# Kernel optimization log

Hardware: AMD Instinct MI355X
Metric: run time of the kernel (lower is better)

Reference implementation:

```python
import jax, jax.numpy as jnp
import numpy as np

B, V, H, R, RULE_DIM, DK, GMLP_H, OUT = 4096, 8, 512, 16, 64, 32, 16, 512
TEMP = float(np.sqrt(DK))  # SelectAttention temperature = sqrt(d_k)
EPS = 1e-10


def gumbel_hard(logits, u, tau=1.0):
    # straight-through hard gumbel-softmax over last axis (F.gumbel_softmax hard=True)
    g = -jnp.log(-jnp.log(u + EPS) + EPS)
    y = jax.nn.softmax((logits + g) / tau, axis=-1)
    hard = jax.nn.one_hot(jnp.argmax(y, axis=-1), y.shape[-1], dtype=y.dtype)
    return hard + y - jax.lax.stop_gradient(y)


def setup_inputs() -> dict:
    key = jax.random.key(0)
    ks = jax.random.split(key, 16)
    s = lambda d: 1.0 / np.sqrt(d)
    return {
        "hidden": jax.random.normal(ks[0], (B, V, H), jnp.float32),
        "u_var": jax.random.uniform(ks[1], (B, V * V), jnp.float32),
        "u_rule": jax.random.uniform(ks[2], (B, R), jnp.float32),
        # variable_rule_select: shared query/key Linear(H, 32)
        "Wq": jax.random.normal(ks[3], (H, DK), jnp.float32) * s(H),
        "bq": jnp.zeros((DK,), jnp.float32),
        "Wk": jax.random.normal(ks[4], (H, DK), jnp.float32) * s(H),
        "bk": jnp.zeros((DK,), jnp.float32),
        # rule embeddings [R, rule_dim]
        "rule_emb": jax.random.normal(ks[5], (R, RULE_DIM), jnp.float32),
        # rule_select_: shared Linear(3H, 32) query, Linear(rule_dim, 32) key
        "Wq2": jax.random.normal(ks[6], (3 * H, DK), jnp.float32) * s(3 * H),
        "bq2": jnp.zeros((DK,), jnp.float32),
        "Wk2": jax.random.normal(ks[7], (RULE_DIM, DK), jnp.float32) * s(RULE_DIM),
        "bk2": jnp.zeros((DK,), jnp.float32),
        # rule_mlp = GroupMLP(2H -> 16 -> input_dim, num=R), GroupLinearLayer has no bias
        "W1": jax.random.normal(ks[8], (R, 2 * H, GMLP_H), jnp.float32) * s(2 * H),
        "W2": jax.random.normal(ks[9], (R, GMLP_H, OUT), jnp.float32) * s(GMLP_H),
    }


def reference(hidden, u_var, u_rule, Wq, bq, Wk, bk, rule_emb, Wq2, bq2, Wk2, bk2, W1, W2):
    b, v, h = hidden.shape
    # variable_rule_select(hidden, hidden): shared Linear projections, bmm scores
    q = hidden @ Wq + bq                                  # [B,V,dk]
    k = hidden @ Wk + bk                                  # [B,V,dk]
    scores = jnp.einsum('bid,bjd->bij', q, k) / TEMP      # [B,V,V]
    # hard gumbel-softmax over flattened V*V pair grid
    mask = gumbel_hard(scores.reshape(b, -1), u_var).reshape(b, v, v)
    mask = mask.transpose(0, 2, 1)                        # mask.permute(0,2,1)
    primary = mask.sum(axis=2)                            # [B,V] one-hot primary variable
    context = mask.sum(axis=1)                            # [B,V] one-hot context variable
    h_p = jnp.einsum('bv,bvh->bh', primary, hidden)       # gather primary slot
    h_c = jnp.einsum('bv,bvh->bh', context, hidden)       # gather context slot
    h_mean = hidden.mean(axis=1)
    # rule_select_: query from concat(primary, context, pooled state) [B,3H]
    q2 = jnp.concatenate([h_p, h_c, h_mean], axis=-1) @ Wq2 + bq2   # [B,dk]
    k2 = rule_emb @ Wk2 + bk2                                        # [R,dk]
    rscores = (q2 @ k2.T) / TEMP                                     # [B,R]
    rmask = gumbel_hard(rscores, u_rule)                             # [B,R] one-hot rule
    # rule_mlp: GroupMLP(2H->16->input_dim) over all rules, then hard dispatch
    comb = jnp.concatenate([h_p, h_c], axis=-1)                      # [B,2H]
    h1 = jax.nn.relu(jnp.einsum('bd,rde->bre', comb, W1))            # [B,R,16]
    rout = jnp.einsum('bre,reo->bro', h1, W2)                        # [B,R,out]
    rule_out = jnp.einsum('br,bro->bo', rmask, rout)                 # [B,out]
    # scatter result back to the selected primary variable slot
    out = primary[:, :, None] * rule_out[:, None, :]                 # [B,V,out]
    return out
```

## Files before the change

### kernel.cpp

```cpp
#include <hip/hip_runtime.h>

#define TEMP 5.656854249492380195f
#define EPSG 1e-10f

#define XSTR 68
#define WSTR 64

__launch_bounds__(256, 2)
__global__ void k1_kernel(const float* __restrict__ hidden,
                          const float* __restrict__ u_var,
                          const float* __restrict__ Wq,
                          const float* __restrict__ bq,
                          const float* __restrict__ Wk,
                          const float* __restrict__ bk,
                          const float* __restrict__ rule_emb,
                          const float* __restrict__ Wk2,
                          const float* __restrict__ bk2,
                          float* __restrict__ k2f,
                          int* __restrict__ selbuf,
                          float* __restrict__ outbuf) {
    const int tid = threadIdx.x;
    const int b0  = blockIdx.x * 8;

    __shared__ float4 smem4[(64 * XSTR + 64 * WSTR) / 4];
    float* smem = reinterpret_cast<float*>(smem4);
    float* xt = smem;
    float* wt = smem + 64 * XSTR;

    if (blockIdx.x == 0) {
        for (int t = tid; t < 512; t += 256) {
            int r = t >> 5, d = t & 31;
            float acc = bk2[d];
            for (int h = 0; h < 64; ++h)
                acc += rule_emb[r * 64 + h] * Wk2[h * 32 + d];
            k2f[t] = acc;
        }
    }

    const int tn = tid & 15;
    const int tm = tid >> 4;

    float4 acc0 = make_float4(0.f, 0.f, 0.f, 0.f);
    float4 acc1 = make_float4(0.f, 0.f, 0.f, 0.f);
    float4 acc2 = make_float4(0.f, 0.f, 0.f, 0.f);
    float4 acc3 = make_float4(0.f, 0.f, 0.f, 0.f);

    for (int c = 0; c < 8; ++c) {
        #pragma unroll
        for (int p = 0; p < 4; ++p) {
            int f   = p * 256 + tid;
            int row = f >> 4;
            int c4  = f & 15;
            int bb  = row >> 3, v = row & 7;
            float4 val = *reinterpret_cast<const float4*>(
                hidden + (size_t)(b0 + bb) * 4096 + v * 512 + c * 64 + c4 * 4);
            *reinterpret_cast<float4*>(&xt[row * XSTR + c4 * 4]) = val;
        }
        #pragma unroll
        for (int p = 0; p < 4; ++p) {
            int f  = p * 256 + tid;
            int k  = f >> 4;
            int n4 = f & 15;
            int h  = c * 64 + k;
            const float* src = (n4 < 8) ? (Wq + h * 32 + n4 * 4)
                                        : (Wk + h * 32 + (n4 - 8) * 4);
            *reinterpret_cast<float4*>(&wt[k * WSTR + n4 * 4]) =
                *reinterpret_cast<const float4*>(src);
        }
        __syncthreads();

        #pragma unroll 4
        for (int k4 = 0; k4 < 16; ++k4) {
            float4 x0 = *reinterpret_cast<const float4*>(&xt[(tm * 4 + 0) * XSTR + k4 * 4]);
            float4 x1 = *reinterpret_cast<const float4*>(&xt[(tm * 4 + 1) * XSTR + k4 * 4]);
            float4 x2 = *reinterpret_cast<const float4*>(&xt[(tm * 4 + 2) * XSTR + k4 * 4]);
            float4 x3 = *reinterpret_cast<const float4*>(&xt[(tm * 4 + 3) * XSTR + k4 * 4]);
            float4 w0 = *reinterpret_cast<const float4*>(&wt[(k4 * 4 + 0) * WSTR + tn * 4]);
            float4 w1 = *reinterpret_cast<const float4*>(&wt[(k4 * 4 + 1) * WSTR + tn * 4]);
            float4 w2 = *reinterpret_cast<const float4*>(&wt[(k4 * 4 + 2) * WSTR + tn * 4]);
            float4 w3 = *reinterpret_cast<const float4*>(&wt[(k4 * 4 + 3) * WSTR + tn * 4]);
            acc0.x += x0.x * w0.x + x0.y * w1.x + x0.z * w2.x + x0.w * w3.x;
            acc0.y += x0.x * w0.y + x0.y * w1.y + x0.z * w2.y + x0.w * w3.y;
            acc0.z += x0.x * w0.z + x0.y * w1.z + x0.z * w2.z + x0.w * w3.z;
            acc0.w += x0.x * w0.w + x0.y * w1.w + x0.z * w2.w + x0.w * w3.w;
            acc1.x += x1.x * w0.x + x1.y * w1.x + x1.z * w2.x + x1.w * w3.x;
            acc1.y += x1.x * w0.y + x1.y * w1.y + x1.z * w2.y + x1.w * w3.y;
            acc1.z += x1.x * w0.z + x1.y * w1.z + x1.z * w2.z + x1.w * w3.z;
            acc1.w += x1.x * w0.w + x1.y * w1.w + x1.z * w2.w + x1.w * w3.w;
            acc2.x += x2.x * w0.x + x2.y * w1.x + x2.z * w2.x + x2.w * w3.x;
            acc2.y += x2.x * w0.y + x2.y * w1.y + x2.z * w2.y + x2.w * w3.y;
            acc2.z += x2.x * w0.z + x2.y * w1.z + x2.z * w2.z + x2.w * w3.z;
            acc2.w += x2.x * w0.w + x2.y * w1.w + x2.z * w2.w + x2.w * w3.w;
            acc3.x += x3.x * w0.x + x3.y * w1.x + x3.z * w2.x + x3.w * w3.x;
            acc3.y += x3.x * w0.y + x3.y * w1.y + x3.z * w2.y + x3.w * w3.y;
            acc3.z += x3.x * w0.z + x3.y * w1.z + x3.z * w2.z + x3.w * w3.z;
            acc3.w += x3.x * w0.w + x3.y * w1.w + x3.z * w2.w + x3.w * w3.w;
        }

        {
            int bb = tid >> 5, hg = tid & 31;
            float m0 = 0.f, m1 = 0.f;
            #pragma unroll
            for (int v = 0; v < 8; ++v) {
                float2 x2 = *reinterpret_cast<const float2*>(&xt[(bb * 8 + v) * XSTR + hg * 2]);
                m0 += x2.x; m1 += x2.y;
            }
            float2 o; o.x = m0 * 0.125f; o.y = m1 * 0.125f;
            *reinterpret_cast<float2*>(outbuf + (size_t)(b0 + bb) * 4096 + c * 64 + hg * 2) = o;
        }
        __syncthreads();
    }

    {
        const float* bsrc = (tn < 8) ? (bq + tn * 4) : (bk + (tn - 8) * 4);
        float4 bias4 = *reinterpret_cast<const float4*>(bsrc);
        float4 r0, r1, r2, r3;
        r0.x = acc0.x + bias4.x; r0.y = acc0.y + bias4.y; r0.z = acc0.z + bias4.z; r0.w = acc0.w + bias4.w;
        r1.x = acc1.x + bias4.x; r1.y = acc1.y + bias4.y; r1.z = acc1.z + bias4.z; r1.w = acc1.w + bias4.w;
        r2.x = acc2.x + bias4.x; r2.y = acc2.y + bias4.y; r2.z = acc2.z + bias4.z; r2.w = acc2.w + bias4.w;
        r3.x = acc3.x + bias4.x; r3.y = acc3.y + bias4.y; r3.z = acc3.z + bias4.z; r3.w = acc3.w + bias4.w;
        float* sq = smem;
        *reinterpret_cast<float4*>(&sq[(tm * 4 + 0) * XSTR + tn * 4]) = r0;
        *reinterpret_cast<float4*>(&sq[(tm * 4 + 1) * XSTR + tn * 4]) = r1;
        *reinterpret_cast<float4*>(&sq[(tm * 4 + 2) * XSTR + tn * 4]) = r2;
        *reinterpret_cast<float4*>(&sq[(tm * 4 + 3) * XSTR + tn * 4]) = r3;
    }
    __syncthreads();

    {
        const float* sq = smem;
        const int w    = tid >> 6;
        const int lane = tid & 63;
        #pragma unroll
        for (int half = 0; half < 2; ++half) {
            const int bb = w + half * 4;
            const int b  = b0 + bb;
            const int i = lane >> 3, j = lane & 7;
            float s = 0.f;
            #pragma unroll
            for (int d4 = 0; d4 < 8; ++d4) {
                float4 qv = *reinterpret_cast<const float4*>(&sq[(bb * 8 + i) * XSTR + d4 * 4]);
                float4 kv = *reinterpret_cast<const float4*>(&sq[(bb * 8 + j) * XSTR + 32 + d4 * 4]);
                s += qv.x * kv.x + qv.y * kv.y + qv.z * kv.z + qv.w * kv.w;
            }
            s /= TEMP;
            float u = u_var[(size_t)b * 64 + lane];
            float g = -logf(-logf(u + EPSG) + EPSG);
            float pm = s + g;
            int idx = lane;
            #pragma unroll
            for (int off = 32; off >= 1; off >>= 1) {
                float pv = __shfl_xor(pm, off);
                int   pi = __shfl_xor(idx, off);
                if (pv > pm || (pv == pm && pi < idx)) { pm = pv; idx = pi; }
            }
            if (lane == 0) selbuf[b] = idx;
        }
    }
}

__launch_bounds__(256, 4)
__global__ void k2sel_kernel(const float* __restrict__ hidden,
                             const float* __restrict__ u_rule,
                             const float* __restrict__ Wq2,
                             const float* __restrict__ bq2,
                             const float* __restrict__ k2f,
                             const int* __restrict__ selbuf,
                             const float* __restrict__ hmeanbuf,
                             int* __restrict__ rselbuf) {
    const int tid = threadIdx.x;
    const int b0 = blockIdx.x * 8;

    __shared__ float  s_k2[512];
    __shared__ float  xt[8][256];
    __shared__ float4 part4[4][8][8];
    __shared__ float  s_q2[8][32];
    __shared__ int    s_sel8[8];

    s_k2[tid]       = k2f[tid];
    s_k2[tid + 256] = k2f[tid + 256];
    if (tid < 8) s_sel8[tid] = selbuf[b0 + tid];
    __syncthreads();

    const int d4 = tid & 7, s = tid >> 3;
    float4 acc[8];
    #pragma unroll
    for (int bb = 0; bb < 8; ++bb) acc[bb] = make_float4(0.f, 0.f, 0.f, 0.f);

    for (int kt = 0; kt < 6; ++kt) {
        float4 w[8];
        #pragma unroll
        for (int j = 0; j < 8; ++j)
            w[j] = *reinterpret_cast<const float4*>(Wq2 + (size_t)(kt * 256 + s * 8 + j) * 32 + d4 * 4);
        #pragma unroll
        for (int bb = 0; bb < 8; ++bb) {
            const int b  = b0 + bb;
            const int sv = s_sel8[bb];
            const float* src;
            if (kt < 2)      src = hidden  + ((size_t)b * 8 + (sv & 7))  * 512 + kt * 256;
            else if (kt < 4) src = hidden  + ((size_t)b * 8 + (sv >> 3)) * 512 + (kt - 2) * 256;
            else             src = hmeanbuf + (size_t)b * 4096 + (kt - 4) * 256;
            xt[bb][tid] = src[tid];
        }
        __syncthreads();
        #pragma unroll
        for (int bb = 0; bb < 8; ++bb) {
            #pragma unroll
            for (int j = 0; j < 8; ++j) {
                float x = xt[bb][s * 8 + j];
                acc[bb].x += x * w[j].x;
                acc[bb].y += x * w[j].y;
                acc[bb].z += x * w[j].z;
                acc[bb].w += x * w[j].w;
            }
        }
        __syncthreads();
    }
    #pragma unroll
    for (int off = 8; off < 64; off <<= 1) {
        #pragma unroll
        for (int bb = 0; bb < 8; ++bb) {
            acc[bb].x += __shfl_xor(acc[bb].x, off);
            acc[bb].y += __shfl_xor(acc[bb].y, off);
            acc[bb].z += __shfl_xor(acc[bb].z, off);
            acc[bb].w += __shfl_xor(acc[bb].w, off);
        }
    }
    if ((s & 7) == 0) {
        #pragma unroll
        for (int bb = 0; bb < 8; ++bb) part4[tid >> 6][bb][d4] = acc[bb];
    }
    __syncthreads();
    {
        const int bb = tid >> 5, col = tid & 31;
        float q2 = bq2[col];
        #pragma unroll
        for (int wv = 0; wv < 4; ++wv) {
            const float* pf = reinterpret_cast<const float*>(&part4[wv][bb][col >> 2]);
            q2 += pf[col & 3];
        }
        s_q2[bb][col] = q2;
    }
    __syncthreads();
    if (tid < 128) {
        const int bb = tid >> 4, r = tid & 15;
        const int b = b0 + bb;
        float sc = 0.f;
        #pragma unroll
        for (int d = 0; d < 32; ++d) sc += s_q2[bb][d] * s_k2[r * 32 + d];
        sc /= TEMP;
        float u = u_rule[(size_t)b * 16 + r];
        float g = -logf(-logf(u + EPSG) + EPSG);
        float pm = sc + g;
        int idx = r;
        #pragma unroll
        for (int off = 8; off >= 1; off >>= 1) {
            float pv = __shfl_xor(pm, off, 16);
            int   pi = __shfl_xor(idx, off, 16);
            if (pv > pm || (pv == pm && pi < idx)) { pm = pv; idx = pi; }
        }
        if (r == 0) rselbuf[b] = idx;
    }
}

__launch_bounds__(256, 4)
__global__ void k3_kernel(const float* __restrict__ hidden,
                          const float* __restrict__ W1,
                          const float* __restrict__ W2,
                          const int* __restrict__ selbuf,
                          const int* __restrict__ rselbuf,
                          float* __restrict__ outbuf) {
    const int tid = threadIdx.x;
    const int b   = blockIdx.x;

    __shared__ float comb[1024];
    __shared__ float part[4][16];
    __shared__ float s_h1[16];
    __shared__ float s_rout[512];

    const int sv = selbuf[b];
    const int r  = rselbuf[b];
    const int js = sv & 7, cs = sv >> 3;

    {
        const float4* h4 = reinterpret_cast<const float4*>(hidden);
        float4 v;
        if (tid < 128) v = h4[((size_t)b * 8 + js) * 128 + tid];
        else           v = h4[((size_t)b * 8 + cs) * 128 + (tid - 128)];
        *reinterpret_cast<float4*>(&comb[tid * 4]) = v;
    }
    __syncthreads();

    {
        const int e  = tid & 15;
        const int sl = tid >> 4;
        const float* w1p = W1 + (size_t)r * 16384;
        float a = 0.f;
        for (int i = 0; i < 64; ++i) {
            int rr = i * 16 + sl;
            a += comb[rr] * w1p[rr * 16 + e];
        }
        a += __shfl_xor(a, 16);
        a += __shfl_xor(a, 32);
        if ((sl & 3) == 0) part[sl >> 2][e] = a;
    }
    __syncthreads();
    if (tid < 16)
        s_h1[tid] = fmaxf(part[0][tid] + part[1][tid] + part[2][tid] + part[3][tid], 0.f);
    __syncthreads();

    {
        const float* w2 = W2 + (size_t)r * 8192;
        int o0 = tid * 2;
        float a0 = 0.f, a1 = 0.f;
        #pragma unroll
        for (int ee = 0; ee < 16; ++ee) {
            float h1e = s_h1[ee];
            float2 ww = *reinterpret_cast<const float2*>(w2 + ee * 512 + o0);
            a0 += h1e * ww.x;
            a1 += h1e * ww.y;
        }
        s_rout[o0]     = a0;
        s_rout[o0 + 1] = a1;
    }
    __syncthreads();

    {
        const int v    = tid >> 5;
        const int col0 = (tid & 31) * 16;
        float4 z = make_float4(0.f, 0.f, 0.f, 0.f);
        float4 r0 = z, r1 = z, r2 = z, r3 = z;
        if (v == js) {
            r0 = *reinterpret_cast<const float4*>(&s_rout[col0]);
            r1 = *reinterpret_cast<const float4*>(&s_rout[col0 + 4]);
            r2 = *reinterpret_cast<const float4*>(&s_rout[col0 + 8]);
            r3 = *reinterpret_cast<const float4*>(&s_rout[col0 + 12]);
        }
        float* ob = outbuf + (size_t)b * 4096 + v * 512 + col0;
        *reinterpret_cast<float4*>(ob)      = r0;
        *reinterpret_cast<float4*>(ob + 4)  = r1;
        *reinterpret_cast<float4*>(ob + 8)  = r2;
        *reinterpret_cast<float4*>(ob + 12) = r3;
    }
}

extern "C" void kernel_launch(void* const* d_in, const int* in_sizes, int n_in,
                              void* d_out, int out_size, void* d_ws, size_t ws_size,
                              hipStream_t stream) {
    const float* hidden   = (const float*)d_in[0];
    const float* u_var    = (const float*)d_in[1];
    const float* u_rule   = (const float*)d_in[2];
    const float* Wq       = (const float*)d_in[3];
    const float* bq       = (const float*)d_in[4];
    const float* Wk       = (const float*)d_in[5];
    const float* bk       = (const float*)d_in[6];
    const float* rule_emb = (const float*)d_in[7];
    const float* Wq2      = (const float*)d_in[8];
    const float* bq2      = (const float*)d_in[9];
    const float* Wk2      = (const float*)d_in[10];
    const float* bk2      = (const float*)d_in[11];
    const float* W1       = (const float*)d_in[12];
    const float* W2       = (const float*)d_in[13];

    char* ws = (char*)d_ws;
    float* k2f  = (float*)(ws);
    int*   sel  = (int*)(ws + 4096);
    int*   rsel = (int*)(ws + 20480);
    float* outf = (float*)d_out;

    hipLaunchKernelGGL(k1_kernel, dim3(512), dim3(256), 0, stream,
                       hidden, u_var, Wq, bq, Wk, bk,
                       rule_emb, Wk2, bk2, k2f, sel, outf);
    hipLaunchKernelGGL(k2sel_kernel, dim3(512), dim3(256), 0, stream,
                       hidden, u_rule, Wq2, bq2, k2f, sel, outf, rsel);
    hipLaunchKernelGGL(k3_kernel, dim3(4096), dim3(256), 0, stream,
                       hidden, W1, W2, sel, rsel, outf);
}
```

Measured before the change: 91.47 us.

## Register-prefetch next tile in k1 and halve batches per block in k2sel

In k1, the global loads for the next 64-wide chunk of hidden and Wq/Wk are issued into registers before the current chunk's FMA loop, then written to shared memory after the barrier, so memory latency overlaps with compute. k2sel now processes 4 batch rows per block instead of 8 and launches twice as many blocks, which raises parallelism across CUs but re-reads the Wq2 weights twice as often. The prefetch adds registers per thread, which may affect occupancy under the launch bounds of 2.

```diff
diff --git a/kernel.cpp b/kernel.cpp
--- a/kernel.cpp
+++ b/kernel.cpp
@@ -40,34 +40,47 @@
     const int tn = tid & 15;
     const int tm = tid >> 4;
 
+    const int srow = tid >> 4;
+    const int sc4  = tid & 15;
+
     float4 acc0 = make_float4(0.f, 0.f, 0.f, 0.f);
     float4 acc1 = make_float4(0.f, 0.f, 0.f, 0.f);
     float4 acc2 = make_float4(0.f, 0.f, 0.f, 0.f);
     float4 acc3 = make_float4(0.f, 0.f, 0.f, 0.f);
 
+    float4 px[4], pw[4];
+
+    #pragma unroll
+    for (int p = 0; p < 4; ++p) {
+        int row = p * 16 + srow;
+        int bb  = row >> 3, v = row & 7;
+        px[p] = *reinterpret_cast<const float4*>(
+            hidden + (size_t)(b0 + bb) * 4096 + v * 512 + 0 * 64 + sc4 * 4);
+        const float* wsrc = (sc4 < 8) ? (Wq + (0 * 64 + row) * 32 + sc4 * 4)
+                                      : (Wk + (0 * 64 + row) * 32 + (sc4 - 8) * 4);
+        pw[p] = *reinterpret_cast<const float4*>(wsrc);
+    }
+    #pragma unroll
+    for (int p = 0; p < 4; ++p) {
+        int row = p * 16 + srow;
+        *reinterpret_cast<float4*>(&xt[row * XSTR + sc4 * 4]) = px[p];
+        *reinterpret_cast<float4*>(&wt[row * WSTR + sc4 * 4]) = pw[p];
+    }
+    __syncthreads();
+
     for (int c = 0; c < 8; ++c) {
-        #pragma unroll
-        for (int p = 0; p < 4; ++p) {
-            int f   = p * 256 + tid;
-            int row = f >> 4;
-            int c4  = f & 15;
-            int bb  = row >> 3, v = row & 7;
-            float4 val = *reinterpret_cast<const float4*>(
-                hidden + (size_t)(b0 + bb) * 4096 + v * 512 + c * 64 + c4 * 4);
-            *reinterpret_cast<float4*>(&xt[row * XSTR + c4 * 4]) = val;
-        }
-        #pragma unroll
-        for (int p = 0; p < 4; ++p) {
-            int f  = p * 256 + tid;
-            int k  = f >> 4;
-            int n4 = f & 15;
-            int h  = c * 64 + k;
-            const float* src = (n4 < 8) ? (Wq + h * 32 + n4 * 4)
-                                        : (Wk + h * 32 + (n4 - 8) * 4);
-            *reinterpret_cast<float4*>(&wt[k * WSTR + n4 * 4]) =
-                *reinterpret_cast<const float4*>(src);
-        }
-        __syncthreads();
+        if (c < 7) {
+            #pragma unroll
+            for (int p = 0; p < 4; ++p) {
+                int row = p * 16 + srow;
+                int bb  = row >> 3, v = row & 7;
+                px[p] = *reinterpret_cast<const float4*>(
+                    hidden + (size_t)(b0 + bb) * 4096 + v * 512 + (c + 1) * 64 + sc4 * 4);
+                const float* wsrc = (sc4 < 8) ? (Wq + ((c + 1) * 64 + row) * 32 + sc4 * 4)
+                                              : (Wk + ((c + 1) * 64 + row) * 32 + (sc4 - 8) * 4);
+                pw[p] = *reinterpret_cast<const float4*>(wsrc);
+            }
+        }
 
         #pragma unroll 4
         for (int k4 = 0; k4 < 16; ++k4) {
@@ -109,6 +122,16 @@
             *reinterpret_cast<float2*>(outbuf + (size_t)(b0 + bb) * 4096 + c * 64 + hg * 2) = o;
         }
         __syncthreads();
+
+        if (c < 7) {
+            #pragma unroll
+            for (int p = 0; p < 4; ++p) {
+                int row = p * 16 + srow;
+                *reinterpret_cast<float4*>(&xt[row * XSTR + sc4 * 4]) = px[p];
+                *reinterpret_cast<float4*>(&wt[row * WSTR + sc4 * 4]) = pw[p];
+            }
+            __syncthreads();
+        }
     }
 
     {
@@ -169,23 +192,23 @@
                              const float* __restrict__ hmeanbuf,
                              int* __restrict__ rselbuf) {
     const int tid = threadIdx.x;
-    const int b0 = blockIdx.x * 8;
+    const int b0 = blockIdx.x * 4;
 
     __shared__ float  s_k2[512];
-    __shared__ float  xt[8][256];
-    __shared__ float4 part4[4][8][8];
-    __shared__ float  s_q2[8][32];
-    __shared__ int    s_sel8[8];
+    __shared__ float  xt[4][256];
+    __shared__ float4 part4[4][4][8];
+    __shared__ float  s_q2[4][32];
+    __shared__ int    s_sel4[4];
 
     s_k2[tid]       = k2f[tid];
     s_k2[tid + 256] = k2f[tid + 256];
-    if (tid < 8) s_sel8[tid] = selbuf[b0 + tid];
+    if (tid < 4) s_sel4[tid] = selbuf[b0 + tid];
     __syncthreads();
 
     const int d4 = tid & 7, s = tid >> 3;
-    float4 acc[8];
+    float4 acc[4];
     #pragma unroll
-    for (int bb = 0; bb < 8; ++bb) acc[bb] = make_float4(0.f, 0.f, 0.f, 0.f);
+    for (int bb = 0; bb < 4; ++bb) acc[bb] = make_float4(0.f, 0.f, 0.f, 0.f);
 
     for (int kt = 0; kt < 6; ++kt) {
         float4 w[8];
@@ -193,9 +216,9 @@
         for (int j = 0; j < 8; ++j)
             w[j] = *reinterpret_cast<const float4*>(Wq2 + (size_t)(kt * 256 + s * 8 + j) * 32 + d4 * 4);
         #pragma unroll
-        for (int bb = 0; bb < 8; ++bb) {
+        for (int bb = 0; bb < 4; ++bb) {
             const int b  = b0 + bb;
-            const int sv = s_sel8[bb];
+            const int sv = s_sel4[bb];
             const float* src;
             if (kt < 2)      src = hidden  + ((size_t)b * 8 + (sv & 7))  * 512 + kt * 256;
             else if (kt < 4) src = hidden  + ((size_t)b * 8 + (sv >> 3)) * 512 + (kt - 2) * 256;
@@ -204,7 +227,7 @@
         }
         __syncthreads();
         #pragma unroll
-        for (int bb = 0; bb < 8; ++bb) {
+        for (int bb = 0; bb < 4; ++bb) {
             #pragma unroll
             for (int j = 0; j < 8; ++j) {
                 float x = xt[bb][s * 8 + j];
@@ -219,7 +242,7 @@
     #pragma unroll
     for (int off = 8; off < 64; off <<= 1) {
         #pragma unroll
-        for (int bb = 0; bb < 8; ++bb) {
+        for (int bb = 0; bb < 4; ++bb) {
             acc[bb].x += __shfl_xor(acc[bb].x, off);
             acc[bb].y += __shfl_xor(acc[bb].y, off);
             acc[bb].z += __shfl_xor(acc[bb].z, off);
@@ -228,10 +251,10 @@
     }
     if ((s & 7) == 0) {
         #pragma unroll
-        for (int bb = 0; bb < 8; ++bb) part4[tid >> 6][bb][d4] = acc[bb];
-    }
-    __syncthreads();
-    {
+        for (int bb = 0; bb < 4; ++bb) part4[tid >> 6][bb][d4] = acc[bb];
+    }
+    __syncthreads();
+    if (tid < 128) {
         const int bb = tid >> 5, col = tid & 31;
         float q2 = bq2[col];
         #pragma unroll
@@ -242,7 +265,7 @@
         s_q2[bb][col] = q2;
     }
     __syncthreads();
-    if (tid < 128) {
+    if (tid < 64) {
         const int bb = tid >> 4, r = tid & 15;
         const int b = b0 + bb;
         float sc = 0.f;
@@ -371,7 +394,7 @@
     hipLaunchKernelGGL(k1_kernel, dim3(512), dim3(256), 0, stream,
                        hidden, u_var, Wq, bq, Wk, bk,
                        rule_emb, Wk2, bk2, k2f, sel, outf);
-    hipLaunchKernelGGL(k2sel_kernel, dim3(512), dim3(256), 0, stream,
+    hipLaunchKernelGGL(k2sel_kernel, dim3(1024), dim3(256), 0, stream,
                        hidden, u_rule, Wq2, bq2, k2f, sel, outf, rsel);
     hipLaunchKernelGGL(k3_kernel, dim3(4096), dim3(256), 0, stream,
                        hidden, W1, W2, sel, rsel, outf);
```

New measurement: 109.4 us. +19.7%, slower.

## Fuse rule selection and rule MLP into one kernel with per-wave batches

Applied to the files above, without the earlier changes.

Merges the rule-selection kernel and the rule-MLP/scatter kernel into a single kernel that processes 4 batch rows per block. The gathered primary/context rows and the mean state are loaded into shared memory once and reused for both the Wq2 projection and the W1 MLP. Each wave then computes one batch's MLP, broadcasting the hidden activations by shuffle instead of shared memory. This removes a launch, the rsel round trip through global memory and the repeated gather of hidden rows. In exchange it uses more shared memory per block, with a lower occupancy bound, and only 4 rows share each Wq2 weight load instead of 8.

```diff
diff --git a/kernel.cpp b/kernel.cpp
--- a/kernel.cpp
+++ b/kernel.cpp
@@ -159,79 +159,99 @@
     }
 }
 
-__launch_bounds__(256, 4)
-__global__ void k2sel_kernel(const float* __restrict__ hidden,
-                             const float* __restrict__ u_rule,
-                             const float* __restrict__ Wq2,
-                             const float* __restrict__ bq2,
-                             const float* __restrict__ k2f,
-                             const int* __restrict__ selbuf,
-                             const float* __restrict__ hmeanbuf,
-                             int* __restrict__ rselbuf) {
+__launch_bounds__(256, 3)
+__global__ void k23_kernel(const float* __restrict__ hidden,
+                           const float* __restrict__ u_rule,
+                           const float* __restrict__ Wq2,
+                           const float* __restrict__ bq2,
+                           const float* __restrict__ k2f,
+                           const int* __restrict__ selbuf,
+                           const float* __restrict__ hmeanbuf,
+                           const float* __restrict__ W1,
+                           const float* __restrict__ W2,
+                           float* __restrict__ outbuf) {
     const int tid = threadIdx.x;
-    const int b0 = blockIdx.x * 8;
+    const int b0  = blockIdx.x * 4;
 
     __shared__ float  s_k2[512];
-    __shared__ float  xt[8][256];
-    __shared__ float4 part4[4][8][8];
-    __shared__ float  s_q2[8][32];
-    __shared__ int    s_sel8[8];
+    __shared__ float  comb[4][1024];
+    __shared__ float  hm[4][512];
+    __shared__ float4 part4[4][4][8];
+    __shared__ float  s_q2[4][32];
+    __shared__ int    s_sel4[4];
+    __shared__ int    s_rsel[4];
 
     s_k2[tid]       = k2f[tid];
     s_k2[tid + 256] = k2f[tid + 256];
-    if (tid < 8) s_sel8[tid] = selbuf[b0 + tid];
-    __syncthreads();
-
-    const int d4 = tid & 7, s = tid >> 3;
-    float4 acc[8];
-    #pragma unroll
-    for (int bb = 0; bb < 8; ++bb) acc[bb] = make_float4(0.f, 0.f, 0.f, 0.f);
-
-    for (int kt = 0; kt < 6; ++kt) {
-        float4 w[8];
-        #pragma unroll
-        for (int j = 0; j < 8; ++j)
-            w[j] = *reinterpret_cast<const float4*>(Wq2 + (size_t)(kt * 256 + s * 8 + j) * 32 + d4 * 4);
-        #pragma unroll
-        for (int bb = 0; bb < 8; ++bb) {
-            const int b  = b0 + bb;
-            const int sv = s_sel8[bb];
-            const float* src;
-            if (kt < 2)      src = hidden  + ((size_t)b * 8 + (sv & 7))  * 512 + kt * 256;
-            else if (kt < 4) src = hidden  + ((size_t)b * 8 + (sv >> 3)) * 512 + (kt - 2) * 256;
-            else             src = hmeanbuf + (size_t)b * 4096 + (kt - 4) * 256;
-            xt[bb][tid] = src[tid];
-        }
-        __syncthreads();
-        #pragma unroll
-        for (int bb = 0; bb < 8; ++bb) {
-            #pragma unroll
-            for (int j = 0; j < 8; ++j) {
-                float x = xt[bb][s * 8 + j];
-                acc[bb].x += x * w[j].x;
-                acc[bb].y += x * w[j].y;
-                acc[bb].z += x * w[j].z;
-                acc[bb].w += x * w[j].w;
-            }
-        }
-        __syncthreads();
-    }
-    #pragma unroll
-    for (int off = 8; off < 64; off <<= 1) {
-        #pragma unroll
-        for (int bb = 0; bb < 8; ++bb) {
-            acc[bb].x += __shfl_xor(acc[bb].x, off);
-            acc[bb].y += __shfl_xor(acc[bb].y, off);
-            acc[bb].z += __shfl_xor(acc[bb].z, off);
-            acc[bb].w += __shfl_xor(acc[bb].w, off);
-        }
-    }
-    if ((s & 7) == 0) {
-        #pragma unroll
-        for (int bb = 0; bb < 8; ++bb) part4[tid >> 6][bb][d4] = acc[bb];
-    }
-    __syncthreads();
-    {
+    if (tid < 4) s_sel4[tid] = selbuf[b0 + tid];
+    __syncthreads();
+
+    {
+        const float4* h4 = reinterpret_cast<const float4*>(hidden);
+        #pragma unroll
+        for (int p = 0; p < 4; ++p) {
+            int f   = p * 256 + tid;
+            int bb  = f >> 8, idx = f & 255;
+            int half = idx >> 7, c = idx & 127;
+            int sv  = s_sel4[bb];
+            int row = half ? (sv >> 3) : (sv & 7);
+            float4 v = h4[((size_t)(b0 + bb) * 8 + row) * 128 + c];
+            *reinterpret_cast<float4*>(&comb[bb][idx * 4]) = v;
+        }
+        #pragma unroll
+        for (int p = 0; p < 2; ++p) {
+            int f  = p * 256 + tid;
+            int bb = f >> 7, c = f & 127;
+            float4 v = *reinterpret_cast<const float4*>(
+                hmeanbuf + (size_t)(b0 + bb) * 4096 + c * 4);
+            *reinterpret_cast<float4*>(&hm[bb][c * 4]) = v;
+        }
+    }
+    __syncthreads();
+
+    {
+        const int d4 = tid & 7, s = tid >> 3;
+        float4 acc[4];
+        #pragma unroll
+        for (int bb = 0; bb < 4; ++bb) acc[bb] = make_float4(0.f, 0.f, 0.f, 0.f);
+
+        for (int kt = 0; kt < 6; ++kt) {
+            float4 w[8];
+            #pragma unroll
+            for (int j = 0; j < 8; ++j)
+                w[j] = *reinterpret_cast<const float4*>(
+                    Wq2 + (size_t)(kt * 256 + s * 8 + j) * 32 + d4 * 4);
+            #pragma unroll
+            for (int bb = 0; bb < 4; ++bb) {
+                const float* xsrc = (kt < 4) ? &comb[bb][kt * 256]
+                                             : &hm[bb][(kt - 4) * 256];
+                #pragma unroll
+                for (int j = 0; j < 8; ++j) {
+                    float x = xsrc[s * 8 + j];
+                    acc[bb].x += x * w[j].x;
+                    acc[bb].y += x * w[j].y;
+                    acc[bb].z += x * w[j].z;
+                    acc[bb].w += x * w[j].w;
+                }
+            }
+        }
+        #pragma unroll
+        for (int off = 8; off < 64; off <<= 1) {
+            #pragma unroll
+            for (int bb = 0; bb < 4; ++bb) {
+                acc[bb].x += __shfl_xor(acc[bb].x, off);
+                acc[bb].y += __shfl_xor(acc[bb].y, off);
+                acc[bb].z += __shfl_xor(acc[bb].z, off);
+                acc[bb].w += __shfl_xor(acc[bb].w, off);
+            }
+        }
+        if ((s & 7) == 0) {
+            #pragma unroll
+            for (int bb = 0; bb < 4; ++bb) part4[tid >> 6][bb][d4] = acc[bb];
+        }
+    }
+    __syncthreads();
+    if (tid < 128) {
         const int bb = tid >> 5, col = tid & 31;
         float q2 = bq2[col];
         #pragma unroll
@@ -242,7 +262,7 @@
         s_q2[bb][col] = q2;
     }
     __syncthreads();
-    if (tid < 128) {
+    if (tid < 64) {
         const int bb = tid >> 4, r = tid & 15;
         const int b = b0 + bb;
         float sc = 0.f;
@@ -259,88 +279,51 @@
             int   pi = __shfl_xor(idx, off, 16);
             if (pv > pm || (pv == pm && pi < idx)) { pm = pv; idx = pi; }
         }
-        if (r == 0) rselbuf[b] = idx;
-    }
-}
-
-__launch_bounds__(256, 4)
-__global__ void k3_kernel(const float* __restrict__ hidden,
-                          const float* __restrict__ W1,
-                          const float* __restrict__ W2,
-                          const int* __restrict__ selbuf,
-                          const int* __restrict__ rselbuf,
-                          float* __restrict__ outbuf) {
-    const int tid = threadIdx.x;
-    const int b   = blockIdx.x;
-
-    __shared__ float comb[1024];
-    __shared__ float part[4][16];
-    __shared__ float s_h1[16];
-    __shared__ float s_rout[512];
-
-    const int sv = selbuf[b];
-    const int r  = rselbuf[b];
-    const int js = sv & 7, cs = sv >> 3;
-
-    {
-        const float4* h4 = reinterpret_cast<const float4*>(hidden);
-        float4 v;
-        if (tid < 128) v = h4[((size_t)b * 8 + js) * 128 + tid];
-        else           v = h4[((size_t)b * 8 + cs) * 128 + (tid - 128)];
-        *reinterpret_cast<float4*>(&comb[tid * 4]) = v;
-    }
-    __syncthreads();
-
-    {
-        const int e  = tid & 15;
-        const int sl = tid >> 4;
+        if (r == 0) s_rsel[bb] = idx;
+    }
+    __syncthreads();
+
+    {
+        const int w    = tid >> 6;
+        const int lane = tid & 63;
+        const int b    = b0 + w;
+        const int sv   = s_sel4[w];
+        const int js   = sv & 7;
+        const int r    = s_rsel[w];
+
+        const int e  = lane & 15;
+        const int sl = lane >> 4;
+        const float* cb  = comb[w];
         const float* w1p = W1 + (size_t)r * 16384;
         float a = 0.f;
-        for (int i = 0; i < 64; ++i) {
-            int rr = i * 16 + sl;
-            a += comb[rr] * w1p[rr * 16 + e];
+        for (int i = 0; i < 256; ++i) {
+            int rr = i * 4 + sl;
+            a += cb[rr] * w1p[rr * 16 + e];
         }
         a += __shfl_xor(a, 16);
         a += __shfl_xor(a, 32);
-        if ((sl & 3) == 0) part[sl >> 2][e] = a;
-    }
-    __syncthreads();
-    if (tid < 16)
-        s_h1[tid] = fmaxf(part[0][tid] + part[1][tid] + part[2][tid] + part[3][tid], 0.f);
-    __syncthreads();
-
-    {
-        const float* w2 = W2 + (size_t)r * 8192;
-        int o0 = tid * 2;
-        float a0 = 0.f, a1 = 0.f;
+        a = fmaxf(a, 0.f);
+
+        const float* w2 = W2 + (size_t)r * 8192 + lane * 8;
+        float4 oA = make_float4(0.f, 0.f, 0.f, 0.f);
+        float4 oB = make_float4(0.f, 0.f, 0.f, 0.f);
         #pragma unroll
         for (int ee = 0; ee < 16; ++ee) {
-            float h1e = s_h1[ee];
-            float2 ww = *reinterpret_cast<const float2*>(w2 + ee * 512 + o0);
-            a0 += h1e * ww.x;
-            a1 += h1e * ww.y;
-        }
-        s_rout[o0]     = a0;
-        s_rout[o0 + 1] = a1;
-    }
-    __syncthreads();
-
-    {
-        const int v    = tid >> 5;
-        const int col0 = (tid & 31) * 16;
+            float he = __shfl(a, ee);
+            float4 wa = *reinterpret_cast<const float4*>(w2 + ee * 512);
+            float4 wb = *reinterpret_cast<const float4*>(w2 + ee * 512 + 4);
+            oA.x += he * wa.x; oA.y += he * wa.y; oA.z += he * wa.z; oA.w += he * wa.w;
+            oB.x += he * wb.x; oB.y += he * wb.y; oB.z += he * wb.z; oB.w += he * wb.w;
+        }
+
         float4 z = make_float4(0.f, 0.f, 0.f, 0.f);
-        float4 r0 = z, r1 = z, r2 = z, r3 = z;
-        if (v == js) {
-            r0 = *reinterpret_cast<const float4*>(&s_rout[col0]);
-            r1 = *reinterpret_cast<const float4*>(&s_rout[col0 + 4]);
-            r2 = *reinterpret_cast<const float4*>(&s_rout[col0 + 8]);
-            r3 = *reinterpret_cast<const float4*>(&s_rout[col0 + 12]);
-        }
-        float* ob = outbuf + (size_t)b * 4096 + v * 512 + col0;
-        *reinterpret_cast<float4*>(ob)      = r0;
-        *reinterpret_cast<float4*>(ob + 4)  = r1;
-        *reinterpret_cast<float4*>(ob + 8)  = r2;
-        *reinterpret_cast<float4*>(ob + 12) = r3;
+        float* ob = outbuf + (size_t)b * 4096 + lane * 8;
+        #pragma unroll
+        for (int v = 0; v < 8; ++v) {
+            bool hit = (v == js);
+            *reinterpret_cast<float4*>(ob + v * 512)     = hit ? oA : z;
+            *reinterpret_cast<float4*>(ob + v * 512 + 4) = hit ? oB : z;
+        }
     }
 }
 
@@ -365,14 +348,11 @@
     char* ws = (char*)d_ws;
     float* k2f  = (float*)(ws);
     int*   sel  = (int*)(ws + 4096);
-    int*   rsel = (int*)(ws + 20480);
     float* outf = (float*)d_out;
 
     hipLaunchKernelGGL(k1_kernel, dim3(512), dim3(256), 0, stream,
                        hidden, u_var, Wq, bq, Wk, bk,
                        rule_emb, Wk2, bk2, k2f, sel, outf);
-    hipLaunchKernelGGL(k2sel_kernel, dim3(512), dim3(256), 0, stream,
-                       hidden, u_rule, Wq2, bq2, k2f, sel, outf, rsel);
-    hipLaunchKernelGGL(k3_kernel, dim3(4096), dim3(256), 0, stream,
-                       hidden, W1, W2, sel, rsel, outf);
+    hipLaunchKernelGGL(k23_kernel, dim3(1024), dim3(256), 0, stream,
+                       hidden, u_rule, Wq2, bq2, k2f, sel, outf, W1, W2, outf);
 }
```

After: 91.53 us. About the same (+0.1%).

## Fuse rule-selection kernel into variable-selection kernel, keep mean and k2 in LDS

Applied to the files above, without the earlier changes.

Merges the second kernel (rule query projection and gumbel rule selection) into the first kernel. The per-batch hidden mean now stays in shared memory instead of going through the output buffer, and every block computes the rule key projection locally instead of block 0 writing it to global memory. This removes one launch and the global round trips for the mean and k2. In exchange, shared memory per block grows by about 20KB, which may lower occupancy, and each block repeats the small k2 computation.

```diff
diff --git a/kernel.cpp b/kernel.cpp
--- a/kernel.cpp
+++ b/kernel.cpp
@@ -9,6 +9,7 @@
 __launch_bounds__(256, 2)
 __global__ void k1_kernel(const float* __restrict__ hidden,
                           const float* __restrict__ u_var,
+                          const float* __restrict__ u_rule,
                           const float* __restrict__ Wq,
                           const float* __restrict__ bq,
                           const float* __restrict__ Wk,
@@ -16,9 +17,10 @@
                           const float* __restrict__ rule_emb,
                           const float* __restrict__ Wk2,
                           const float* __restrict__ bk2,
-                          float* __restrict__ k2f,
+                          const float* __restrict__ Wq2,
+                          const float* __restrict__ bq2,
                           int* __restrict__ selbuf,
-                          float* __restrict__ outbuf) {
+                          int* __restrict__ rselbuf) {
     const int tid = threadIdx.x;
     const int b0  = blockIdx.x * 8;
 
@@ -26,15 +28,18 @@
     float* smem = reinterpret_cast<float*>(smem4);
     float* xt = smem;
     float* wt = smem + 64 * XSTR;
-
-    if (blockIdx.x == 0) {
-        for (int t = tid; t < 512; t += 256) {
-            int r = t >> 5, d = t & 31;
-            float acc = bk2[d];
-            for (int h = 0; h < 64; ++h)
-                acc += rule_emb[r * 64 + h] * Wk2[h * 32 + d];
-            k2f[t] = acc;
-        }
+    __shared__ float  hm[8 * 512];
+    __shared__ float  sk2[512];
+    __shared__ float4 part4[4][8][8];
+    __shared__ float  s_q2[8][32];
+    __shared__ int    ssel[8];
+
+    for (int t = tid; t < 512; t += 256) {
+        int r = t >> 5, d = t & 31;
+        float acc = bk2[d];
+        for (int h = 0; h < 64; ++h)
+            acc += rule_emb[r * 64 + h] * Wk2[h * 32 + d];
+        sk2[t] = acc;
     }
 
     const int tn = tid & 15;
@@ -105,8 +110,8 @@
                 float2 x2 = *reinterpret_cast<const float2*>(&xt[(bb * 8 + v) * XSTR + hg * 2]);
                 m0 += x2.x; m1 += x2.y;
             }
-            float2 o; o.x = m0 * 0.125f; o.y = m1 * 0.125f;
-            *reinterpret_cast<float2*>(outbuf + (size_t)(b0 + bb) * 4096 + c * 64 + hg * 2) = o;
+            hm[bb * 512 + c * 64 + hg * 2]     = m0 * 0.125f;
+            hm[bb * 512 + c * 64 + hg * 2 + 1] = m1 * 0.125f;
         }
         __syncthreads();
     }
@@ -154,81 +159,68 @@
                 int   pi = __shfl_xor(idx, off);
                 if (pv > pm || (pv == pm && pi < idx)) { pm = pv; idx = pi; }
             }
-            if (lane == 0) selbuf[b] = idx;
-        }
-    }
-}
-
-__launch_bounds__(256, 4)
-__global__ void k2sel_kernel(const float* __restrict__ hidden,
-                             const float* __restrict__ u_rule,
-                             const float* __restrict__ Wq2,
-                             const float* __restrict__ bq2,
-                             const float* __restrict__ k2f,
-                             const int* __restrict__ selbuf,
-                             const float* __restrict__ hmeanbuf,
-                             int* __restrict__ rselbuf) {
-    const int tid = threadIdx.x;
-    const int b0 = blockIdx.x * 8;
-
-    __shared__ float  s_k2[512];
-    __shared__ float  xt[8][256];
-    __shared__ float4 part4[4][8][8];
-    __shared__ float  s_q2[8][32];
-    __shared__ int    s_sel8[8];
-
-    s_k2[tid]       = k2f[tid];
-    s_k2[tid + 256] = k2f[tid + 256];
-    if (tid < 8) s_sel8[tid] = selbuf[b0 + tid];
-    __syncthreads();
-
-    const int d4 = tid & 7, s = tid >> 3;
-    float4 acc[8];
-    #pragma unroll
-    for (int bb = 0; bb < 8; ++bb) acc[bb] = make_float4(0.f, 0.f, 0.f, 0.f);
-
-    for (int kt = 0; kt < 6; ++kt) {
-        float4 w[8];
-        #pragma unroll
-        for (int j = 0; j < 8; ++j)
-            w[j] = *reinterpret_cast<const float4*>(Wq2 + (size_t)(kt * 256 + s * 8 + j) * 32 + d4 * 4);
-        #pragma unroll
-        for (int bb = 0; bb < 8; ++bb) {
-            const int b  = b0 + bb;
-            const int sv = s_sel8[bb];
-            const float* src;
-            if (kt < 2)      src = hidden  + ((size_t)b * 8 + (sv & 7))  * 512 + kt * 256;
-            else if (kt < 4) src = hidden  + ((size_t)b * 8 + (sv >> 3)) * 512 + (kt - 2) * 256;
-            else             src = hmeanbuf + (size_t)b * 4096 + (kt - 4) * 256;
-            xt[bb][tid] = src[tid];
-        }
-        __syncthreads();
-        #pragma unroll
-        for (int bb = 0; bb < 8; ++bb) {
-            #pragma unroll
-            for (int j = 0; j < 8; ++j) {
-                float x = xt[bb][s * 8 + j];
-                acc[bb].x += x * w[j].x;
-                acc[bb].y += x * w[j].y;
-                acc[bb].z += x * w[j].z;
-                acc[bb].w += x * w[j].w;
-            }
-        }
-        __syncthreads();
-    }
-    #pragma unroll
-    for (int off = 8; off < 64; off <<= 1) {
-        #pragma unroll
-        for (int bb = 0; bb < 8; ++bb) {
-            acc[bb].x += __shfl_xor(acc[bb].x, off);
-            acc[bb].y += __shfl_xor(acc[bb].y, off);
-            acc[bb].z += __shfl_xor(acc[bb].z, off);
-            acc[bb].w += __shfl_xor(acc[bb].w, off);
-        }
-    }
-    if ((s & 7) == 0) {
-        #pragma unroll
-        for (int bb = 0; bb < 8; ++bb) part4[tid >> 6][bb][d4] = acc[bb];
+            if (lane == 0) { selbuf[b] = idx; ssel[bb] = idx; }
+        }
+    }
+    __syncthreads();
+
+    {
+        float* comb = smem;
+        const float4* h4 = reinterpret_cast<const float4*>(hidden);
+        #pragma unroll
+        for (int p = 0; p < 8; ++p) {
+            int f    = p * 256 + tid;
+            int bb   = f >> 8, idx = f & 255;
+            int half = idx >> 7, cc = idx & 127;
+            int sv   = ssel[bb];
+            int row  = half ? (sv >> 3) : (sv & 7);
+            reinterpret_cast<float4*>(comb)[bb * 256 + idx] =
+                h4[((size_t)(b0 + bb) * 8 + row) * 128 + cc];
+        }
+    }
+    __syncthreads();
+
+    {
+        const float* comb = smem;
+        const int d4 = tid & 7, s = tid >> 3;
+        float4 acc[8];
+        #pragma unroll
+        for (int bb = 0; bb < 8; ++bb) acc[bb] = make_float4(0.f, 0.f, 0.f, 0.f);
+
+        for (int kt = 0; kt < 6; ++kt) {
+            float4 w[8];
+            #pragma unroll
+            for (int j = 0; j < 8; ++j)
+                w[j] = *reinterpret_cast<const float4*>(
+                    Wq2 + (size_t)(kt * 256 + s * 8 + j) * 32 + d4 * 4);
+            #pragma unroll
+            for (int bb = 0; bb < 8; ++bb) {
+                const float* xsrc = (kt < 4) ? &comb[bb * 1024 + kt * 256]
+                                             : &hm[bb * 512 + (kt - 4) * 256];
+                #pragma unroll
+                for (int j = 0; j < 8; ++j) {
+                    float x = xsrc[s * 8 + j];
+                    acc[bb].x += x * w[j].x;
+                    acc[bb].y += x * w[j].y;
+                    acc[bb].z += x * w[j].z;
+                    acc[bb].w += x * w[j].w;
+                }
+            }
+        }
+        #pragma unroll
+        for (int off = 8; off < 64; off <<= 1) {
+            #pragma unroll
+            for (int bb = 0; bb < 8; ++bb) {
+                acc[bb].x += __shfl_xor(acc[bb].x, off);
+                acc[bb].y += __shfl_xor(acc[bb].y, off);
+                acc[bb].z += __shfl_xor(acc[bb].z, off);
+                acc[bb].w += __shfl_xor(acc[bb].w, off);
+            }
+        }
+        if ((s & 7) == 0) {
+            #pragma unroll
+            for (int bb = 0; bb < 8; ++bb) part4[tid >> 6][bb][d4] = acc[bb];
+        }
     }
     __syncthreads();
     {
@@ -247,7 +239,7 @@
         const int b = b0 + bb;
         float sc = 0.f;
         #pragma unroll
-        for (int d = 0; d < 32; ++d) sc += s_q2[bb][d] * s_k2[r * 32 + d];
+        for (int d = 0; d < 32; ++d) sc += s_q2[bb][d] * sk2[r * 32 + d];
         sc /= TEMP;
         float u = u_rule[(size_t)b * 16 + r];
         float g = -logf(-logf(u + EPSG) + EPSG);
@@ -363,16 +355,13 @@
     const float* W2       = (const float*)d_in[13];
 
     char* ws = (char*)d_ws;
-    float* k2f  = (float*)(ws);
     int*   sel  = (int*)(ws + 4096);
     int*   rsel = (int*)(ws + 20480);
     float* outf = (float*)d_out;
 
     hipLaunchKernelGGL(k1_kernel, dim3(512), dim3(256), 0, stream,
-                       hidden, u_var, Wq, bq, Wk, bk,
-                       rule_emb, Wk2, bk2, k2f, sel, outf);
-    hipLaunchKernelGGL(k2sel_kernel, dim3(512), dim3(256), 0, stream,
-                       hidden, u_rule, Wq2, bq2, k2f, sel, outf, rsel);
+                       hidden, u_var, u_rule, Wq, bq, Wk, bk,
+                       rule_emb, Wk2, bk2, Wq2, bq2, sel, rsel);
     hipLaunchKernelGGL(k3_kernel, dim3(4096), dim3(256), 0, stream,
                        hidden, W1, W2, sel, rsel, outf);
 }
```

Result: no change. 90.39 us (-1.2%).
